# Optimization experiments

Measured on AMD Instinct MI355X. Metric: run time of the kernel, lower is better.

The kernel has to match this reference:

```python
import jax, jax.numpy as jnp
import numpy as np

H = 2048          # hidden_size
IM = 1024         # moe_intermediate_size
E = 16            # n_routed_experts
K = 8             # num_experts_per_tok
N_SHARED = 2      # n_shared_experts
IS = IM * N_SHARED  # shared expert intermediate
B, L = 1, 2048
SCALE = 2.5       # routed_scaling_factor
W_INIT = 0.02


def setup_inputs() -> dict:
    key = jax.random.key(0)
    ks = jax.random.split(key, 9)
    return {
        "hidden_states": jax.random.normal(ks[0], (B, L, H), jnp.float32),
        "gate_w": jax.random.normal(ks[1], (E, H), jnp.float32) * W_INIT,
        "Wg": jax.random.normal(ks[2], (E, H, IM), jnp.float32) * W_INIT,
        "Wu": jax.random.normal(ks[3], (E, H, IM), jnp.float32) * W_INIT,
        "Wd": jax.random.normal(ks[4], (E, IM, H), jnp.float32) * W_INIT,
        "sWg": jax.random.normal(ks[5], (H, IS), jnp.float32) * W_INIT,
        "sWu": jax.random.normal(ks[6], (H, IS), jnp.float32) * W_INIT,
        "sWd": jax.random.normal(ks[7], (IS, H), jnp.float32) * W_INIT,
    }


def reference(hidden_states, gate_w, Wg, Wu, Wd, sWg, sWu, sWd):
    orig_shape = hidden_states.shape
    h = hidden_states.reshape(-1, H)                      # [T, H]
    T = h.shape[0]

    # shared expert (SwiGLU MLP)
    shared = (jax.nn.silu(h @ sWg) * (h @ sWu)) @ sWd     # [T, H]

    # sigmoid router + top-k gating
    router_logits = h @ gate_w.T                          # [T, E]
    routing_weights = jax.nn.sigmoid(router_logits)
    topk_w, topk_idx = jax.lax.top_k(routing_weights, K)  # [T, K]
    topk_w = topk_w / (jnp.sum(topk_w, axis=-1, keepdims=True) + 1e-6)
    topk_w = topk_w * SCALE

    # dense [T, E] combine weights (zero for unselected experts)
    comb = jnp.zeros((T, E), h.dtype).at[jnp.arange(T)[:, None], topk_idx].add(topk_w)

    # all-expert SwiGLU MLP (batched over experts), then weighted combine
    g = jnp.einsum("th,ehi->eti", h, Wg)                  # [E, T, IM]
    u = jnp.einsum("th,ehi->eti", h, Wu)
    eo = jnp.einsum("eti,eih->eth", jax.nn.silu(g) * u, Wd)  # [E, T, H]
    routed = jnp.einsum("eth,te->th", eo, comb)           # [T, H]

    return (shared + routed).reshape(orig_shape)
```

## Files before the change

### kernel.cpp

```cpp
#include <hip/hip_runtime.h>
#include <hip/hip_bf16.h>
#include <stdint.h>

#define H_DIM  2048
#define IM_DIM 1024
#define E_NUM  16
#define TOPK   8
#define IS_DIM 2048
#define SCALE_F 2.5f

#define BM 128
#define BN 128
#define BK 32
#define LDSP 40

typedef __attribute__((ext_vector_type(8))) short   short8;
typedef __attribute__((ext_vector_type(8))) __bf16  bf16x8;
typedef __attribute__((ext_vector_type(4))) float   float4v;
typedef unsigned short ushort_t;

#define GLOAD_LDS16(gp, lp) \
    __builtin_amdgcn_global_load_lds((__attribute__((address_space(1))) void*)(gp), \
                                     (__attribute__((address_space(3))) void*)(lp), 16, 0, 0)

static __device__ __forceinline__ ushort_t f2bf(float x) {
    union { float f; uint32_t u; } v; v.f = x;
    uint32_t r = v.u + 0x7fffu + ((v.u >> 16) & 1u);
    return (ushort_t)(r >> 16);
}

__global__ void cast_h_kernel(const float* __restrict__ h, ushort_t* __restrict__ hb, int n4) {
    int i = blockIdx.x * blockDim.x + threadIdx.x;
    if (i < n4) {
        float4 v = ((const float4*)h)[i];
        ushort4 o;
        o.x = f2bf(v.x); o.y = f2bf(v.y); o.z = f2bf(v.z); o.w = f2bf(v.w);
        ((ushort4*)hb)[i] = o;
    }
}

__global__ void router_kernel(const float* __restrict__ h, const float* __restrict__ gw,
                              float* __restrict__ comb, int T) {
    int t = blockIdx.x;
    int l = threadIdx.x;
    const float* hr = h + (size_t)t * H_DIM;
    __shared__ float logits[E_NUM];
    for (int e = 0; e < E_NUM; e++) {
        const float* g = gw + e * H_DIM;
        float p = 0.f;
        #pragma unroll 8
        for (int j = l; j < H_DIM; j += 64) p += hr[j] * g[j];
        #pragma unroll
        for (int off = 32; off > 0; off >>= 1) p += __shfl_down(p, off);
        if (l == 0) logits[e] = p;
    }
    __syncthreads();
    if (l == 0) {
        float sig[E_NUM]; bool sel[E_NUM];
        #pragma unroll
        for (int e = 0; e < E_NUM; e++) { sig[e] = 1.f / (1.f + expf(-logits[e])); sel[e] = false; }
        #pragma unroll
        for (int k = 0; k < TOPK; k++) {
            int bi = 0; float bv = -1.f;
            #pragma unroll
            for (int e = 0; e < E_NUM; e++)
                if (!sel[e] && sig[e] > bv) { bv = sig[e]; bi = e; }
            sel[bi] = true;
        }
        float s = 0.f;
        #pragma unroll
        for (int e = 0; e < E_NUM; e++) if (sel[e]) s += sig[e];
        float inv = SCALE_F / (s + 1e-6f);
        #pragma unroll
        for (int e = 0; e < E_NUM; e++)
            comb[(size_t)t * E_NUM + e] = sel[e] ? sig[e] * inv : 0.f;
    }
}

__global__ __launch_bounds__(512)
void transpose_cvt_kernel(const float* __restrict__ Sg, const float* __restrict__ Su,
                          ushort_t* __restrict__ Dg, ushort_t* __restrict__ Du,
                          int K, int N, size_t sStride, size_t dStride, int dual)
{
    __shared__ float lds[256][65];

    const int z  = blockIdx.z;
    const int k0 = blockIdx.x * 64;
    const int n0 = blockIdx.y * 256;
    const int tid = threadIdx.x;
    const int rr = tid >> 6;
    const int c4 = (tid & 63) * 4;
    const int n  = tid >> 1;
    const int hh = (tid & 1) * 32;

    for (int m = 0; m < 2; ++m) {
        if (m == 1 && !dual) break;
        const float* S = (m == 0 ? Sg : Su) + (size_t)z * sStride;
        ushort_t*    D = (m == 0 ? Dg : Du) + (size_t)z * dStride;

        if (m == 1) __syncthreads();
        #pragma unroll
        for (int p = 0; p < 8; ++p) {
            int r = p * 8 + rr;
            float4 v = *(const float4*)&S[(size_t)(k0 + r) * N + n0 + c4];
            lds[c4 + 0][r] = v.x;
            lds[c4 + 1][r] = v.y;
            lds[c4 + 2][r] = v.z;
            lds[c4 + 3][r] = v.w;
        }
        __syncthreads();

        ushort_t* drow = &D[(size_t)(n0 + n) * K + k0 + hh];
        #pragma unroll
        for (int q = 0; q < 4; ++q) {
            short8 o;
            #pragma unroll
            for (int j = 0; j < 8; ++j) o[j] = (short)f2bf(lds[n][hh + q * 8 + j]);
            *(short8*)&drow[q * 8] = o;
        }
    }
}


__global__ __launch_bounds__(256, 2)
void gemm1f_kernel(const ushort_t* __restrict__ A, int lda,
                   const ushort_t* __restrict__ Bg0, const ushort_t* __restrict__ Bu0,
                   size_t bSeg,
                   ushort_t* __restrict__ C0, size_t cSeg, int ldc,
                   const float* __restrict__ comb, int Kdim)
{
    __shared__ ushort_t Als[BM * BK];
    __shared__ ushort_t Bgs[BN * BK];
    __shared__ ushort_t Bus[BN * BK];

    int z = blockIdx.z;
    const ushort_t* Bg = Bg0 + (size_t)z * bSeg;
    const ushort_t* Bu = Bu0 + (size_t)z * bSeg;
    ushort_t* C = C0 + (size_t)z * cSeg;
    int t0 = blockIdx.x * BM, n0 = blockIdx.y * BN;
    int tid = threadIdx.x, lane = tid & 63, wid = tid >> 6;
    int wm = (wid & 1) * 64, wn = (wid >> 1) * 64;
    int quad = lane >> 4, l15 = lane & 15;

    int srow = lane >> 2;
    int scol = (lane & 3) * 8;
    int rb = wid * 32;

    float4v accg[4][4], accu[4][4];
    #pragma unroll
    for (int i = 0; i < 4; i++)
        #pragma unroll
        for (int j = 0; j < 4; j++) {
            accg[i][j] = (float4v){0.f, 0.f, 0.f, 0.f};
            accu[i][j] = (float4v){0.f, 0.f, 0.f, 0.f};
        }

    const ushort_t* Ab0  = A  + (size_t)(t0 + rb + srow)      * lda  + scol;
    const ushort_t* Ab1  = A  + (size_t)(t0 + rb + 16 + srow) * lda  + scol;
    const ushort_t* Bgb0 = Bg + (size_t)(n0 + rb + srow)      * Kdim + scol;
    const ushort_t* Bgb1 = Bg + (size_t)(n0 + rb + 16 + srow) * Kdim + scol;
    const ushort_t* Bub0 = Bu + (size_t)(n0 + rb + srow)      * Kdim + scol;
    const ushort_t* Bub1 = Bu + (size_t)(n0 + rb + 16 + srow) * Kdim + scol;
    ushort_t* lA0  = &Als[rb * BK];
    ushort_t* lA1  = &Als[(rb + 16) * BK];
    ushort_t* lBg0 = &Bgs[rb * BK];
    ushort_t* lBg1 = &Bgs[(rb + 16) * BK];
    ushort_t* lBu0 = &Bus[rb * BK];
    ushort_t* lBu1 = &Bus[(rb + 16) * BK];

    for (int k0 = 0; k0 < Kdim; k0 += BK) {
        GLOAD_LDS16(Ab0 + k0,  lA0);
        GLOAD_LDS16(Ab1 + k0,  lA1);
        GLOAD_LDS16(Bgb0 + k0, lBg0);
        GLOAD_LDS16(Bgb1 + k0, lBg1);
        GLOAD_LDS16(Bub0 + k0, lBu0);
        GLOAD_LDS16(Bub1 + k0, lBu1);
        __syncthreads();

        bf16x8 af[4], bg[4], bu[4];
        #pragma unroll
        for (int i = 0; i < 4; i++)
            af[i] = *(const bf16x8*)&Als[(wm + i * 16 + l15) * BK + quad * 8];
        #pragma unroll
        for (int j = 0; j < 4; j++) {
            bg[j] = *(const bf16x8*)&Bgs[(wn + j * 16 + l15) * BK + quad * 8];
            bu[j] = *(const bf16x8*)&Bus[(wn + j * 16 + l15) * BK + quad * 8];
        }
        #pragma unroll
        for (int i = 0; i < 4; i++)
            #pragma unroll
            for (int j = 0; j < 4; j++) {
                accg[i][j] = __builtin_amdgcn_mfma_f32_16x16x32_bf16(af[i], bg[j], accg[i][j], 0, 0, 0);
                accu[i][j] = __builtin_amdgcn_mfma_f32_16x16x32_bf16(af[i], bu[j], accu[i][j], 0, 0, 0);
            }
        __syncthreads();
    }

    #pragma unroll
    for (int i = 0; i < 4; i++) {
        #pragma unroll
        for (int r = 0; r < 4; r++) {
            int t = t0 + wm + i * 16 + quad * 4 + r;
            float sc = comb ? comb[(size_t)t * E_NUM + z] : 1.f;
            #pragma unroll
            for (int j = 0; j < 4; j++) {
                float g = accg[i][j][r], u = accu[i][j][r];
                float sg = g / (1.f + __expf(-g));
                float v = sg * u * sc;
                int c = n0 + wn + j * 16 + l15;
                C[(size_t)t * ldc + c] = f2bf(v);
            }
        }
    }
}

__global__ __launch_bounds__(256, 2)
void gemm2f_kernel(const ushort_t* __restrict__ A0, size_t aSeg, int lda,
                   const ushort_t* __restrict__ B0, size_t bSeg,
                   float* __restrict__ Out, int N,
                   int nsegPerZ, int Kper, int mode)
{
    __shared__ ushort_t Als[BM * BK];
    __shared__ ushort_t Bls[BN * BK];

    int t0 = blockIdx.x * BM, n0 = blockIdx.y * BN;
    int z = blockIdx.z;
    int tid = threadIdx.x, lane = tid & 63, wid = tid >> 6;
    int wm = (wid & 1) * 64, wn = (wid >> 1) * 64;
    int quad = lane >> 4, l15 = lane & 15;

    int srow = lane >> 2;
    int scol = (lane & 3) * 8;
    int rb = wid * 32;

    float4v acc[4][4];
    #pragma unroll
    for (int i = 0; i < 4; i++)
        #pragma unroll
        for (int j = 0; j < 4; j++) acc[i][j] = (float4v){0.f, 0.f, 0.f, 0.f};

    ushort_t* lA0 = &Als[rb * BK];
    ushort_t* lA1 = &Als[(rb + 16) * BK];
    ushort_t* lB0 = &Bls[rb * BK];
    ushort_t* lB1 = &Bls[(rb + 16) * BK];

    for (int s = 0; s < nsegPerZ; s++) {
        int seg = z * nsegPerZ + s;
        const ushort_t* A = A0 + (size_t)seg * aSeg;
        const ushort_t* B = B0 + (size_t)seg * bSeg;
        const ushort_t* Ab0 = A + (size_t)(t0 + rb + srow)      * lda  + scol;
        const ushort_t* Ab1 = A + (size_t)(t0 + rb + 16 + srow) * lda  + scol;
        const ushort_t* Bb0 = B + (size_t)(n0 + rb + srow)      * Kper + scol;
        const ushort_t* Bb1 = B + (size_t)(n0 + rb + 16 + srow) * Kper + scol;

        for (int k0 = 0; k0 < Kper; k0 += BK) {
            GLOAD_LDS16(Ab0 + k0, lA0);
            GLOAD_LDS16(Ab1 + k0, lA1);
            GLOAD_LDS16(Bb0 + k0, lB0);
            GLOAD_LDS16(Bb1 + k0, lB1);
            __syncthreads();

            bf16x8 af[4], bf[4];
            #pragma unroll
            for (int i = 0; i < 4; i++)
                af[i] = *(const bf16x8*)&Als[(wm + i * 16 + l15) * BK + quad * 8];
            #pragma unroll
            for (int j = 0; j < 4; j++)
                bf[j] = *(const bf16x8*)&Bls[(wn + j * 16 + l15) * BK + quad * 8];
            #pragma unroll
            for (int i = 0; i < 4; i++)
                #pragma unroll
                for (int j = 0; j < 4; j++)
                    acc[i][j] = __builtin_amdgcn_mfma_f32_16x16x32_bf16(af[i], bf[j], acc[i][j], 0, 0, 0);
            __syncthreads();
        }
    }

    #pragma unroll
    for (int i = 0; i < 4; i++) {
        #pragma unroll
        for (int r = 0; r < 4; r++) {
            int t = t0 + wm + i * 16 + quad * 4 + r;
            #pragma unroll
            for (int j = 0; j < 4; j++) {
                int c = n0 + wn + j * 16 + l15;
                size_t idx = (size_t)t * N + c;
                float v = acc[i][j][r];
                if (mode == 0) Out[idx] = v;
                else if (mode == 1) Out[idx] += v;
                else atomicAdd(&Out[idx], v);
            }
        }
    }
}


__global__ __launch_bounds__(256)
void gemm1_kernel(const ushort_t* __restrict__ A, int lda,
                  const float* __restrict__ Bg0, const float* __restrict__ Bu0,
                  size_t bSeg, int ldb,
                  ushort_t* __restrict__ C0, size_t cSeg, int ldc,
                  const float* __restrict__ comb, int Kdim)
{
    __shared__ ushort_t Als[BM * LDSP];
    __shared__ ushort_t Bgs[BN * LDSP];
    __shared__ ushort_t Bus[BN * LDSP];

    int z = blockIdx.z;
    const float* Bg = Bg0 + (size_t)z * bSeg;
    const float* Bu = Bu0 + (size_t)z * bSeg;
    ushort_t* C = C0 + (size_t)z * cSeg;

    int t0 = blockIdx.x * BM;
    int n0 = blockIdx.y * BN;
    int tid = threadIdx.x;
    int lane = tid & 63, wid = tid >> 6;
    int wm = (wid & 1) * 64, wn = (wid >> 1) * 64;
    int quad = lane >> 4, l15 = lane & 15;

    float4v accg[4][4], accu[4][4];
    #pragma unroll
    for (int i = 0; i < 4; i++)
        #pragma unroll
        for (int j = 0; j < 4; j++) {
            accg[i][j] = (float4v){0.f, 0.f, 0.f, 0.f};
            accu[i][j] = (float4v){0.f, 0.f, 0.f, 0.f};
        }

    int a_r  = tid >> 2, a_oc = tid & 3;
    int b_ko = (tid >> 4) & 3;
    int b_n  = 2 * ((tid & 15) + ((tid >> 6) << 4));

    for (int k0 = 0; k0 < Kdim; k0 += BK) {
        __syncthreads();
        {
            const ushort_t* s0 = A + (size_t)(t0 + a_r) * lda + k0 + a_oc * 8;
            *(short8*)&Als[a_r * LDSP + a_oc * 8] = *(const short8*)s0;
            const ushort_t* s1 = A + (size_t)(t0 + a_r + 64) * lda + k0 + a_oc * 8;
            *(short8*)&Als[(a_r + 64) * LDSP + a_oc * 8] = *(const short8*)s1;
        }
        {
            short8 g0, g1, u0, u1;
            #pragma unroll
            for (int j = 0; j < 8; j++) {
                size_t roff = (size_t)(k0 + b_ko * 8 + j) * ldb + n0 + b_n;
                float2 vg = *(const float2*)&Bg[roff];
                float2 vu = *(const float2*)&Bu[roff];
                g0[j] = (short)f2bf(vg.x); g1[j] = (short)f2bf(vg.y);
                u0[j] = (short)f2bf(vu.x); u1[j] = (short)f2bf(vu.y);
            }
            *(short8*)&Bgs[b_n * LDSP + b_ko * 8]       = g0;
            *(short8*)&Bgs[(b_n + 1) * LDSP + b_ko * 8] = g1;
            *(short8*)&Bus[b_n * LDSP + b_ko * 8]       = u0;
            *(short8*)&Bus[(b_n + 1) * LDSP + b_ko * 8] = u1;
        }
        __syncthreads();

        bf16x8 af[4], bg[4], bu[4];
        #pragma unroll
        for (int i = 0; i < 4; i++)
            af[i] = *(const bf16x8*)&Als[(wm + i * 16 + l15) * LDSP + quad * 8];
        #pragma unroll
        for (int j = 0; j < 4; j++) {
            bg[j] = *(const bf16x8*)&Bgs[(wn + j * 16 + l15) * LDSP + quad * 8];
            bu[j] = *(const bf16x8*)&Bus[(wn + j * 16 + l15) * LDSP + quad * 8];
        }
        #pragma unroll
        for (int i = 0; i < 4; i++)
            #pragma unroll
            for (int j = 0; j < 4; j++) {
                accg[i][j] = __builtin_amdgcn_mfma_f32_16x16x32_bf16(af[i], bg[j], accg[i][j], 0, 0, 0);
                accu[i][j] = __builtin_amdgcn_mfma_f32_16x16x32_bf16(af[i], bu[j], accu[i][j], 0, 0, 0);
            }
    }

    #pragma unroll
    for (int i = 0; i < 4; i++) {
        #pragma unroll
        for (int r = 0; r < 4; r++) {
            int t = t0 + wm + i * 16 + quad * 4 + r;
            float sc = comb ? comb[(size_t)t * E_NUM + z] : 1.f;
            #pragma unroll
            for (int j = 0; j < 4; j++) {
                float g = accg[i][j][r], u = accu[i][j][r];
                float sg = g / (1.f + __expf(-g));
                float v = sg * u * sc;
                int c = n0 + wn + j * 16 + l15;
                C[(size_t)t * ldc + c] = f2bf(v);
            }
        }
    }
}

__global__ __launch_bounds__(256)
void gemm2_kernel(const ushort_t* __restrict__ A0, size_t aSeg, int lda,
                  const float* __restrict__ B0, size_t bSeg, int ldb,
                  float* __restrict__ Out, int N,
                  int nseg, int Kper, int accum)
{
    __shared__ ushort_t Als[BM * LDSP];
    __shared__ ushort_t Bls[BN * LDSP];

    int t0 = blockIdx.x * BM;
    int n0 = blockIdx.y * BN;
    int tid = threadIdx.x;
    int lane = tid & 63, wid = tid >> 6;
    int wm = (wid & 1) * 64, wn = (wid >> 1) * 64;
    int quad = lane >> 4, l15 = lane & 15;

    float4v acc[4][4];
    #pragma unroll
    for (int i = 0; i < 4; i++)
        #pragma unroll
        for (int j = 0; j < 4; j++) acc[i][j] = (float4v){0.f, 0.f, 0.f, 0.f};

    int a_r  = tid >> 2, a_oc = tid & 3;
    int b_ko = (tid >> 4) & 3;
    int b_n  = 2 * ((tid & 15) + ((tid >> 6) << 4));

    for (int seg = 0; seg < nseg; seg++) {
        const ushort_t* A = A0 + (size_t)seg * aSeg;
        const float*    B = B0 + (size_t)seg * bSeg;
        for (int k0 = 0; k0 < Kper; k0 += BK) {
            __syncthreads();
            {
                const ushort_t* s0 = A + (size_t)(t0 + a_r) * lda + k0 + a_oc * 8;
                *(short8*)&Als[a_r * LDSP + a_oc * 8] = *(const short8*)s0;
                const ushort_t* s1 = A + (size_t)(t0 + a_r + 64) * lda + k0 + a_oc * 8;
                *(short8*)&Als[(a_r + 64) * LDSP + a_oc * 8] = *(const short8*)s1;
            }
            {
                short8 r0, r1;
                #pragma unroll
                for (int j = 0; j < 8; j++) {
                    size_t roff = (size_t)(k0 + b_ko * 8 + j) * ldb + n0 + b_n;
                    float2 v = *(const float2*)&B[roff];
                    r0[j] = (short)f2bf(v.x); r1[j] = (short)f2bf(v.y);
                }
                *(short8*)&Bls[b_n * LDSP + b_ko * 8]       = r0;
                *(short8*)&Bls[(b_n + 1) * LDSP + b_ko * 8] = r1;
            }
            __syncthreads();

            bf16x8 af[4], bf[4];
            #pragma unroll
            for (int i = 0; i < 4; i++)
                af[i] = *(const bf16x8*)&Als[(wm + i * 16 + l15) * LDSP + quad * 8];
            #pragma unroll
            for (int j = 0; j < 4; j++)
                bf[j] = *(const bf16x8*)&Bls[(wn + j * 16 + l15) * LDSP + quad * 8];
            #pragma unroll
            for (int i = 0; i < 4; i++)
                #pragma unroll
                for (int j = 0; j < 4; j++)
                    acc[i][j] = __builtin_amdgcn_mfma_f32_16x16x32_bf16(af[i], bf[j], acc[i][j], 0, 0, 0);
        }
    }

    #pragma unroll
    for (int i = 0; i < 4; i++) {
        #pragma unroll
        for (int r = 0; r < 4; r++) {
            int t = t0 + wm + i * 16 + quad * 4 + r;
            #pragma unroll
            for (int j = 0; j < 4; j++) {
                int c = n0 + wn + j * 16 + l15;
                size_t idx = (size_t)t * N + c;
                float v = acc[i][j][r];
                if (accum) Out[idx] += v; else Out[idx] = v;
            }
        }
    }
}


extern "C" void kernel_launch(void* const* d_in, const int* in_sizes, int n_in,
                              void* d_out, int out_size, void* d_ws, size_t ws_size,
                              hipStream_t stream) {
    const float* h      = (const float*)d_in[0];
    const float* gate_w = (const float*)d_in[1];
    const float* Wg     = (const float*)d_in[2];
    const float* Wu     = (const float*)d_in[3];
    const float* Wd     = (const float*)d_in[4];
    const float* sWg    = (const float*)d_in[5];
    const float* sWu    = (const float*)d_in[6];
    const float* sWd    = (const float*)d_in[7];
    float* out = (float*)d_out;
    int T = in_sizes[0] / H_DIM;
    (void)n_in; (void)out_size;

    char* ws = (char*)d_ws;
    size_t off = 0;
    auto alloc = [&](size_t bytes) -> void* {
        void* p = ws + off;
        off = (off + bytes + 255) & ~(size_t)255;
        return p;
    };
    ushort_t* h_bf  = (ushort_t*)alloc((size_t)T * H_DIM * 2);
    float*    comb  = (float*)   alloc((size_t)T * E_NUM * 4);
    ushort_t* act_s = (ushort_t*)alloc((size_t)T * IS_DIM * 2);
    ushort_t* act_r = (ushort_t*)alloc((size_t)E_NUM * T * IM_DIM * 2);
    ushort_t* bufS1 = (ushort_t*)alloc((size_t)IS_DIM * H_DIM * 2);
    ushort_t* bufS2 = (ushort_t*)alloc((size_t)IS_DIM * H_DIM * 2);
    ushort_t* bufW1 = (ushort_t*)alloc((size_t)E_NUM * IM_DIM * H_DIM * 2);
    ushort_t* bufW2 = (ushort_t*)alloc((size_t)E_NUM * IM_DIM * H_DIM * 2);
    size_t need = off;

    int n4 = T * H_DIM / 4;
    cast_h_kernel<<<(n4 + 255) / 256, 256, 0, stream>>>(h, h_bf, n4);
    router_kernel<<<T, 64, 0, stream>>>(h, gate_w, comb, T);

    if (ws_size >= need) {
        transpose_cvt_kernel<<<dim3(H_DIM / 64, IS_DIM / 256, 1), 512, 0, stream>>>(
            sWg, sWu, bufS1, bufS2, H_DIM, IS_DIM, 0, 0, 1);
        gemm1f_kernel<<<dim3(T / BM, IS_DIM / BN, 1), 256, 0, stream>>>(
            h_bf, H_DIM, bufS1, bufS2, 0, act_s, 0, IS_DIM, nullptr, H_DIM);

        transpose_cvt_kernel<<<dim3(H_DIM / 64, IM_DIM / 256, E_NUM), 512, 0, stream>>>(
            Wg, Wu, bufW1, bufW2, H_DIM, IM_DIM,
            (size_t)H_DIM * IM_DIM, (size_t)IM_DIM * H_DIM, 1);
        gemm1f_kernel<<<dim3(T / BM, IM_DIM / BN, E_NUM), 256, 0, stream>>>(
            h_bf, H_DIM, bufW1, bufW2, (size_t)IM_DIM * H_DIM,
            act_r, (size_t)T * IM_DIM, IM_DIM, comb, H_DIM);

        transpose_cvt_kernel<<<dim3(IS_DIM / 64, H_DIM / 256, 1), 512, 0, stream>>>(
            sWd, nullptr, bufS1, nullptr, IS_DIM, H_DIM, 0, 0, 0);
        gemm2f_kernel<<<dim3(T / BM, H_DIM / BN, 1), 256, 0, stream>>>(
            act_s, 0, IS_DIM, bufS1, 0, out, H_DIM, 1, IS_DIM, 0);

        transpose_cvt_kernel<<<dim3(IM_DIM / 64, H_DIM / 256, E_NUM), 512, 0, stream>>>(
            Wd, nullptr, bufW1, nullptr, IM_DIM, H_DIM,
            (size_t)IM_DIM * H_DIM, (size_t)H_DIM * IM_DIM, 0);
        gemm2f_kernel<<<dim3(T / BM, H_DIM / BN, 2), 256, 0, stream>>>(
            act_r, (size_t)T * IM_DIM, IM_DIM, bufW1, (size_t)H_DIM * IM_DIM,
            out, H_DIM, E_NUM / 2, IM_DIM, 2);
    } else {
        gemm1_kernel<<<dim3(T / BM, IS_DIM / BN, 1), 256, 0, stream>>>(
            h_bf, H_DIM, sWg, sWu, 0, IS_DIM, act_s, 0, IS_DIM, nullptr, H_DIM);
        gemm1_kernel<<<dim3(T / BM, IM_DIM / BN, E_NUM), 256, 0, stream>>>(
            h_bf, H_DIM, Wg, Wu, (size_t)H_DIM * IM_DIM, IM_DIM,
            act_r, (size_t)T * IM_DIM, IM_DIM, comb, H_DIM);
        gemm2_kernel<<<dim3(T / BM, H_DIM / BN, 1), 256, 0, stream>>>(
            act_s, 0, IS_DIM, sWd, 0, H_DIM, out, H_DIM, 1, IS_DIM, 0);
        gemm2_kernel<<<dim3(T / BM, H_DIM / BN, 1), 256, 0, stream>>>(
            act_r, (size_t)T * IM_DIM, IM_DIM, Wd, (size_t)IM_DIM * H_DIM, H_DIM,
            out, H_DIM, E_NUM, IM_DIM, 1);
    }
}
```

Before: 1.154 ms.

## Merge shared and routed expert launches into unified transpose and GEMM kernels

The shared expert is treated as two extra IM-wide expert slices, so the gate/up transpose, the gate/up GEMM, the down transpose and the down GEMM each run as a single launch over E+2 z-slices instead of separate shared and routed launches. The output is zeroed inside the cast kernel, and all down-projection results are accumulated with atomics. This cuts the number of kernel launches and fills the GPU better by running the small shared-expert GEMMs alongside the routed ones. In exchange, the shared expert's output now goes through atomic adds instead of a direct store, and the cast kernel writes extra bytes to zero the output.

```diff
diff --git a/kernel.cpp b/kernel.cpp
--- a/kernel.cpp
+++ b/kernel.cpp
@@ -29,13 +29,15 @@
     return (ushort_t)(r >> 16);
 }
 
-__global__ void cast_h_kernel(const float* __restrict__ h, ushort_t* __restrict__ hb, int n4) {
+__global__ void cast_zero_kernel(const float* __restrict__ h, ushort_t* __restrict__ hb,
+                                 float4* __restrict__ outz, int n4) {
     int i = blockIdx.x * blockDim.x + threadIdx.x;
     if (i < n4) {
         float4 v = ((const float4*)h)[i];
         ushort4 o;
         o.x = f2bf(v.x); o.y = f2bf(v.y); o.z = f2bf(v.z); o.w = f2bf(v.w);
         ((ushort4*)hb)[i] = o;
+        outz[i] = make_float4(0.f, 0.f, 0.f, 0.f);
     }
 }
 
@@ -77,66 +79,119 @@
     }
 }
 
-__global__ __launch_bounds__(512)
-void transpose_cvt_kernel(const float* __restrict__ Sg, const float* __restrict__ Su,
-                          ushort_t* __restrict__ Dg, ushort_t* __restrict__ Du,
-                          int K, int N, size_t sStride, size_t dStride, int dual)
-{
-    __shared__ float lds[256][65];
-
-    const int z  = blockIdx.z;
-    const int k0 = blockIdx.x * 64;
-    const int n0 = blockIdx.y * 256;
-    const int tid = threadIdx.x;
+static __device__ __forceinline__
+void transpose_body(const float* __restrict__ S, ushort_t* __restrict__ D,
+                    int srcLd, int dstLd, int k0, int n0, int tid,
+                    float (*lds)[65])
+{
     const int rr = tid >> 6;
     const int c4 = (tid & 63) * 4;
     const int n  = tid >> 1;
     const int hh = (tid & 1) * 32;
 
-    for (int m = 0; m < 2; ++m) {
-        if (m == 1 && !dual) break;
-        const float* S = (m == 0 ? Sg : Su) + (size_t)z * sStride;
-        ushort_t*    D = (m == 0 ? Dg : Du) + (size_t)z * dStride;
-
-        if (m == 1) __syncthreads();
-        #pragma unroll
-        for (int p = 0; p < 8; ++p) {
-            int r = p * 8 + rr;
-            float4 v = *(const float4*)&S[(size_t)(k0 + r) * N + n0 + c4];
-            lds[c4 + 0][r] = v.x;
-            lds[c4 + 1][r] = v.y;
-            lds[c4 + 2][r] = v.z;
-            lds[c4 + 3][r] = v.w;
-        }
-        __syncthreads();
-
-        ushort_t* drow = &D[(size_t)(n0 + n) * K + k0 + hh];
-        #pragma unroll
-        for (int q = 0; q < 4; ++q) {
-            short8 o;
-            #pragma unroll
-            for (int j = 0; j < 8; ++j) o[j] = (short)f2bf(lds[n][hh + q * 8 + j]);
-            *(short8*)&drow[q * 8] = o;
-        }
-    }
-}
-
+    #pragma unroll
+    for (int p = 0; p < 8; ++p) {
+        int r = p * 8 + rr;
+        float4 v = *(const float4*)&S[(size_t)(k0 + r) * srcLd + n0 + c4];
+        lds[c4 + 0][r] = v.x;
+        lds[c4 + 1][r] = v.y;
+        lds[c4 + 2][r] = v.z;
+        lds[c4 + 3][r] = v.w;
+    }
+    __syncthreads();
+
+    ushort_t* drow = &D[(size_t)(n0 + n) * dstLd + k0 + hh];
+    #pragma unroll
+    for (int q = 0; q < 4; ++q) {
+        short8 o;
+        #pragma unroll
+        for (int j = 0; j < 8; ++j) o[j] = (short)f2bf(lds[n][hh + q * 8 + j]);
+        *(short8*)&drow[q * 8] = o;
+    }
+}
+
+__global__ __launch_bounds__(512)
+void transpose_gu_kernel(const float* __restrict__ Wg, const float* __restrict__ Wu,
+                         const float* __restrict__ sWg, const float* __restrict__ sWu,
+                         ushort_t* __restrict__ bufW1, ushort_t* __restrict__ bufW2,
+                         ushort_t* __restrict__ bufS1, ushort_t* __restrict__ bufS2)
+{
+    __shared__ float lds[256][65];
+    const int z = blockIdx.z;
+    const int k0 = blockIdx.x * 64;
+    const int n0 = blockIdx.y * 256;
+    const int tid = threadIdx.x;
+
+    const float* Sg; const float* Su; ushort_t* Dg; ushort_t* Du; int srcLd;
+    if (z < E_NUM) {
+        Sg = Wg + (size_t)z * H_DIM * IM_DIM;
+        Su = Wu + (size_t)z * H_DIM * IM_DIM;
+        Dg = bufW1 + (size_t)z * IM_DIM * H_DIM;
+        Du = bufW2 + (size_t)z * IM_DIM * H_DIM;
+        srcLd = IM_DIM;
+    } else {
+        int s = z - E_NUM;
+        Sg = sWg + (size_t)s * IM_DIM;
+        Su = sWu + (size_t)s * IM_DIM;
+        Dg = bufS1 + (size_t)s * IM_DIM * H_DIM;
+        Du = bufS2 + (size_t)s * IM_DIM * H_DIM;
+        srcLd = IS_DIM;
+    }
+    transpose_body(Sg, Dg, srcLd, H_DIM, k0, n0, tid, lds);
+    __syncthreads();
+    transpose_body(Su, Du, srcLd, H_DIM, k0, n0, tid, lds);
+}
+
+__global__ __launch_bounds__(512)
+void transpose_d_kernel(const float* __restrict__ Wd, const float* __restrict__ sWd,
+                        ushort_t* __restrict__ bufW2, ushort_t* __restrict__ bufS2)
+{
+    __shared__ float lds[256][65];
+    const int z = blockIdx.z;
+    const int k0 = blockIdx.x * 64;
+    const int n0 = blockIdx.y * 256;
+    const int tid = threadIdx.x;
+
+    const float* S; ushort_t* D; int dstLd;
+    if (z < E_NUM) {
+        S = Wd + (size_t)z * IM_DIM * H_DIM;
+        D = bufW2 + (size_t)z * H_DIM * IM_DIM;
+        dstLd = IM_DIM;
+    } else {
+        int s = z - E_NUM;
+        S = sWd + (size_t)s * IM_DIM * H_DIM;
+        D = bufS2 + (size_t)s * IM_DIM;
+        dstLd = IS_DIM;
+    }
+    transpose_body(S, D, H_DIM, dstLd, k0, n0, tid, lds);
+}
 
 __global__ __launch_bounds__(256, 2)
-void gemm1f_kernel(const ushort_t* __restrict__ A, int lda,
-                   const ushort_t* __restrict__ Bg0, const ushort_t* __restrict__ Bu0,
-                   size_t bSeg,
-                   ushort_t* __restrict__ C0, size_t cSeg, int ldc,
-                   const float* __restrict__ comb, int Kdim)
+void gemm1u_kernel(const ushort_t* __restrict__ A,
+                   const ushort_t* __restrict__ bufW1, const ushort_t* __restrict__ bufW2,
+                   const ushort_t* __restrict__ bufS1, const ushort_t* __restrict__ bufS2,
+                   ushort_t* __restrict__ act_r, ushort_t* __restrict__ act_s,
+                   const float* __restrict__ comb, int T)
 {
     __shared__ ushort_t Als[BM * BK];
     __shared__ ushort_t Bgs[BN * BK];
     __shared__ ushort_t Bus[BN * BK];
 
-    int z = blockIdx.z;
-    const ushort_t* Bg = Bg0 + (size_t)z * bSeg;
-    const ushort_t* Bu = Bu0 + (size_t)z * bSeg;
-    ushort_t* C = C0 + (size_t)z * cSeg;
+    const int z = blockIdx.z;
+    const ushort_t* Bg; const ushort_t* Bu; ushort_t* C; int ldc; bool useComb;
+    if (z < E_NUM) {
+        Bg = bufW1 + (size_t)z * IM_DIM * H_DIM;
+        Bu = bufW2 + (size_t)z * IM_DIM * H_DIM;
+        C  = act_r + (size_t)z * T * IM_DIM;
+        ldc = IM_DIM; useComb = true;
+    } else {
+        int s = z - E_NUM;
+        Bg = bufS1 + (size_t)s * IM_DIM * H_DIM;
+        Bu = bufS2 + (size_t)s * IM_DIM * H_DIM;
+        C  = act_s + (size_t)s * IM_DIM;
+        ldc = IS_DIM; useComb = false;
+    }
+
     int t0 = blockIdx.x * BM, n0 = blockIdx.y * BN;
     int tid = threadIdx.x, lane = tid & 63, wid = tid >> 6;
     int wm = (wid & 1) * 64, wn = (wid >> 1) * 64;
@@ -155,12 +210,12 @@
             accu[i][j] = (float4v){0.f, 0.f, 0.f, 0.f};
         }
 
-    const ushort_t* Ab0  = A  + (size_t)(t0 + rb + srow)      * lda  + scol;
-    const ushort_t* Ab1  = A  + (size_t)(t0 + rb + 16 + srow) * lda  + scol;
-    const ushort_t* Bgb0 = Bg + (size_t)(n0 + rb + srow)      * Kdim + scol;
-    const ushort_t* Bgb1 = Bg + (size_t)(n0 + rb + 16 + srow) * Kdim + scol;
-    const ushort_t* Bub0 = Bu + (size_t)(n0 + rb + srow)      * Kdim + scol;
-    const ushort_t* Bub1 = Bu + (size_t)(n0 + rb + 16 + srow) * Kdim + scol;
+    const ushort_t* Ab0  = A  + (size_t)(t0 + rb + srow)      * H_DIM + scol;
+    const ushort_t* Ab1  = A  + (size_t)(t0 + rb + 16 + srow) * H_DIM + scol;
+    const ushort_t* Bgb0 = Bg + (size_t)(n0 + rb + srow)      * H_DIM + scol;
+    const ushort_t* Bgb1 = Bg + (size_t)(n0 + rb + 16 + srow) * H_DIM + scol;
+    const ushort_t* Bub0 = Bu + (size_t)(n0 + rb + srow)      * H_DIM + scol;
+    const ushort_t* Bub1 = Bu + (size_t)(n0 + rb + 16 + srow) * H_DIM + scol;
     ushort_t* lA0  = &Als[rb * BK];
     ushort_t* lA1  = &Als[(rb + 16) * BK];
     ushort_t* lBg0 = &Bgs[rb * BK];
@@ -168,7 +223,7 @@
     ushort_t* lBu0 = &Bus[rb * BK];
     ushort_t* lBu1 = &Bus[(rb + 16) * BK];
 
-    for (int k0 = 0; k0 < Kdim; k0 += BK) {
+    for (int k0 = 0; k0 < H_DIM; k0 += BK) {
         GLOAD_LDS16(Ab0 + k0,  lA0);
         GLOAD_LDS16(Ab1 + k0,  lA1);
         GLOAD_LDS16(Bgb0 + k0, lBg0);
@@ -201,7 +256,7 @@
         #pragma unroll
         for (int r = 0; r < 4; r++) {
             int t = t0 + wm + i * 16 + quad * 4 + r;
-            float sc = comb ? comb[(size_t)t * E_NUM + z] : 1.f;
+            float sc = useComb ? comb[(size_t)t * E_NUM + z] : 1.f;
             #pragma unroll
             for (int j = 0; j < 4; j++) {
                 float g = accg[i][j][r], u = accu[i][j][r];
@@ -215,10 +270,9 @@
 }
 
 __global__ __launch_bounds__(256, 2)
-void gemm2f_kernel(const ushort_t* __restrict__ A0, size_t aSeg, int lda,
-                   const ushort_t* __restrict__ B0, size_t bSeg,
-                   float* __restrict__ Out, int N,
-                   int nsegPerZ, int Kper, int mode)
+void gemm2u_kernel(const ushort_t* __restrict__ act_r, const ushort_t* __restrict__ act_s,
+                   const ushort_t* __restrict__ bufW2, const ushort_t* __restrict__ bufS2,
+                   float* __restrict__ Out, int T, int nsegPerZ)
 {
     __shared__ ushort_t Als[BM * BK];
     __shared__ ushort_t Bls[BN * BK];
@@ -246,14 +300,21 @@
 
     for (int s = 0; s < nsegPerZ; s++) {
         int seg = z * nsegPerZ + s;
-        const ushort_t* A = A0 + (size_t)seg * aSeg;
-        const ushort_t* B = B0 + (size_t)seg * bSeg;
-        const ushort_t* Ab0 = A + (size_t)(t0 + rb + srow)      * lda  + scol;
-        const ushort_t* Ab1 = A + (size_t)(t0 + rb + 16 + srow) * lda  + scol;
-        const ushort_t* Bb0 = B + (size_t)(n0 + rb + srow)      * Kper + scol;
-        const ushort_t* Bb1 = B + (size_t)(n0 + rb + 16 + srow) * Kper + scol;
-
-        for (int k0 = 0; k0 < Kper; k0 += BK) {
+        const ushort_t* A; const ushort_t* B; int lda, ldb;
+        if (seg < E_NUM) {
+            A = act_r + (size_t)seg * T * IM_DIM;  lda = IM_DIM;
+            B = bufW2 + (size_t)seg * H_DIM * IM_DIM; ldb = IM_DIM;
+        } else {
+            int s2 = seg - E_NUM;
+            A = act_s + (size_t)s2 * IM_DIM;  lda = IS_DIM;
+            B = bufS2 + (size_t)s2 * IM_DIM;  ldb = IS_DIM;
+        }
+        const ushort_t* Ab0 = A + (size_t)(t0 + rb + srow)      * lda + scol;
+        const ushort_t* Ab1 = A + (size_t)(t0 + rb + 16 + srow) * lda + scol;
+        const ushort_t* Bb0 = B + (size_t)(n0 + rb + srow)      * ldb + scol;
+        const ushort_t* Bb1 = B + (size_t)(n0 + rb + 16 + srow) * ldb + scol;
+
+        for (int k0 = 0; k0 < IM_DIM; k0 += BK) {
             GLOAD_LDS16(Ab0 + k0, lA0);
             GLOAD_LDS16(Ab1 + k0, lA1);
             GLOAD_LDS16(Bb0 + k0, lB0);
@@ -284,11 +345,7 @@
             #pragma unroll
             for (int j = 0; j < 4; j++) {
                 int c = n0 + wn + j * 16 + l15;
-                size_t idx = (size_t)t * N + c;
-                float v = acc[i][j][r];
-                if (mode == 0) Out[idx] = v;
-                else if (mode == 1) Out[idx] += v;
-                else atomicAdd(&Out[idx], v);
+                atomicAdd(&Out[(size_t)t * H_DIM + c], acc[i][j][r]);
             }
         }
     }
@@ -507,41 +564,32 @@
     size_t need = off;
 
     int n4 = T * H_DIM / 4;
-    cast_h_kernel<<<(n4 + 255) / 256, 256, 0, stream>>>(h, h_bf, n4);
-    router_kernel<<<T, 64, 0, stream>>>(h, gate_w, comb, T);
 
     if (ws_size >= need) {
-        transpose_cvt_kernel<<<dim3(H_DIM / 64, IS_DIM / 256, 1), 512, 0, stream>>>(
-            sWg, sWu, bufS1, bufS2, H_DIM, IS_DIM, 0, 0, 1);
-        gemm1f_kernel<<<dim3(T / BM, IS_DIM / BN, 1), 256, 0, stream>>>(
-            h_bf, H_DIM, bufS1, bufS2, 0, act_s, 0, IS_DIM, nullptr, H_DIM);
-
-        transpose_cvt_kernel<<<dim3(H_DIM / 64, IM_DIM / 256, E_NUM), 512, 0, stream>>>(
-            Wg, Wu, bufW1, bufW2, H_DIM, IM_DIM,
-            (size_t)H_DIM * IM_DIM, (size_t)IM_DIM * H_DIM, 1);
-        gemm1f_kernel<<<dim3(T / BM, IM_DIM / BN, E_NUM), 256, 0, stream>>>(
-            h_bf, H_DIM, bufW1, bufW2, (size_t)IM_DIM * H_DIM,
-            act_r, (size_t)T * IM_DIM, IM_DIM, comb, H_DIM);
-
-        transpose_cvt_kernel<<<dim3(IS_DIM / 64, H_DIM / 256, 1), 512, 0, stream>>>(
-            sWd, nullptr, bufS1, nullptr, IS_DIM, H_DIM, 0, 0, 0);
-        gemm2f_kernel<<<dim3(T / BM, H_DIM / BN, 1), 256, 0, stream>>>(
-            act_s, 0, IS_DIM, bufS1, 0, out, H_DIM, 1, IS_DIM, 0);
-
-        transpose_cvt_kernel<<<dim3(IM_DIM / 64, H_DIM / 256, E_NUM), 512, 0, stream>>>(
-            Wd, nullptr, bufW1, nullptr, IM_DIM, H_DIM,
-            (size_t)IM_DIM * H_DIM, (size_t)H_DIM * IM_DIM, 0);
-        gemm2f_kernel<<<dim3(T / BM, H_DIM / BN, 2), 256, 0, stream>>>(
-            act_r, (size_t)T * IM_DIM, IM_DIM, bufW1, (size_t)H_DIM * IM_DIM,
-            out, H_DIM, E_NUM / 2, IM_DIM, 2);
+        cast_zero_kernel<<<(n4 + 255) / 256, 256, 0, stream>>>(h, h_bf, (float4*)out, n4);
+        router_kernel<<<T, 64, 0, stream>>>(h, gate_w, comb, T);
+
+        transpose_gu_kernel<<<dim3(H_DIM / 64, IM_DIM / 256, E_NUM + 2), 512, 0, stream>>>(
+            Wg, Wu, sWg, sWu, bufW1, bufW2, bufS1, bufS2);
+
+        gemm1u_kernel<<<dim3(T / BM, IM_DIM / BN, E_NUM + 2), 256, 0, stream>>>(
+            h_bf, bufW1, bufW2, bufS1, bufS2, act_r, act_s, comb, T);
+
+        transpose_d_kernel<<<dim3(IM_DIM / 64, H_DIM / 256, E_NUM + 2), 512, 0, stream>>>(
+            Wd, sWd, bufW2, bufS2);
+
+        gemm2u_kernel<<<dim3(T / BM, H_DIM / BN, 2), 256, 0, stream>>>(
+            act_r, act_s, bufW2, bufS2, out, T, (E_NUM + 2) / 2);
     } else {
+        cast_zero_kernel<<<(n4 + 255) / 256, 256, 0, stream>>>(h, h_bf, (float4*)out, n4);
+        router_kernel<<<T, 64, 0, stream>>>(h, gate_w, comb, T);
         gemm1_kernel<<<dim3(T / BM, IS_DIM / BN, 1), 256, 0, stream>>>(
             h_bf, H_DIM, sWg, sWu, 0, IS_DIM, act_s, 0, IS_DIM, nullptr, H_DIM);
         gemm1_kernel<<<dim3(T / BM, IM_DIM / BN, E_NUM), 256, 0, stream>>>(
             h_bf, H_DIM, Wg, Wu, (size_t)H_DIM * IM_DIM, IM_DIM,
             act_r, (size_t)T * IM_DIM, IM_DIM, comb, H_DIM);
         gemm2_kernel<<<dim3(T / BM, H_DIM / BN, 1), 256, 0, stream>>>(
-            act_s, 0, IS_DIM, sWd, 0, H_DIM, out, H_DIM, 1, IS_DIM, 0);
+            act_s, 0, IS_DIM, sWd, 0, H_DIM, out, H_DIM, 1, IS_DIM, 1);
         gemm2_kernel<<<dim3(T / BM, H_DIM / BN, 1), 256, 0, stream>>>(
             act_r, (size_t)T * IM_DIM, IM_DIM, Wd, (size_t)IM_DIM * H_DIM, H_DIM,
             out, H_DIM, E_NUM, IM_DIM, 1);
```

New measurement: 1.111 ms. -3.8%, faster.
